# Kernel optimization log

Measured on AMD Instinct MI355X. Metric: run time of the kernel, lower is better.

## Reference

```python
import jax, jax.numpy as jnp
import numpy as np

B, S, D, H = 4, 2048, 1024, 16
HD = D // H
EPS = 1e-5
MASKED_BIAS = -10000.0

def setup_inputs() -> dict:
    key = jax.random.key(0)
    ks = jax.random.split(key, 12)
    sd = 0.02
    return {
        "hidden_states": jax.random.normal(ks[0], (B, S, D), jnp.float32),
        "Wq": jax.random.normal(ks[1], (D, D), jnp.float32) * sd,
        "bq": jnp.zeros((D,), jnp.float32),
        "Wk": jax.random.normal(ks[2], (D, D), jnp.float32) * sd,
        "bk": jnp.zeros((D,), jnp.float32),
        "Wv": jax.random.normal(ks[3], (D, D), jnp.float32) * sd,
        "bv": jnp.zeros((D,), jnp.float32),
        "Wp": jax.random.normal(ks[4], (D, D), jnp.float32) * sd,
        "bp": jnp.zeros((D,), jnp.float32),
        "ln_g": jnp.ones((D,), jnp.float32),
        "ln_b": jnp.zeros((D,), jnp.float32),
    }

def reference(hidden_states, Wq, bq, Wk, bk, Wv, bv, Wp, bp, ln_g, ln_b):
    x = hidden_states  # [B,S,D]
    # QKV projections (nn.Linear: x @ W^T + b; here W stored as [D,D], use x@W)
    q = x @ Wq + bq
    k = x @ Wk + bk
    v = x @ Wv + bv
    # split heads -> [B,H,S,HD]
    def split(t):
        return t.reshape(B, S, H, HD).transpose(0, 2, 1, 3)
    q, k, v = split(q), split(k), split(v)
    # scaled scores [B,H,S,S]
    scores = jnp.einsum("bhqd,bhkd->bhqk", q, k) / jnp.float32(np.sqrt(HD))
    causal = jnp.tril(jnp.ones((S, S), bool))
    scores = jnp.where(causal[None, None], scores, jnp.float32(MASKED_BIAS))
    attn = jax.nn.softmax(scores, axis=-1)
    out = jnp.einsum("bhqk,bhkd->bhqd", attn, v)
    # merge heads -> [B,S,D]
    out = out.transpose(0, 2, 1, 3).reshape(B, S, D)
    out = out @ Wp + bp
    # residual + layernorm
    y = out + x
    mu = jnp.mean(y, axis=-1, keepdims=True)
    var = jnp.var(y, axis=-1, keepdims=True)
    y = (y - mu) * jax.lax.rsqrt(var + EPS) * ln_g + ln_b
    return y
```

## Files before the change

kernel.cpp:

```cpp
#include <hip/hip_runtime.h>
#include <math.h>

#define B_  4
#define S_  2048
#define D_  1024
#define H_  16
#define HD_ 64
#define M_  (B_*S_)

typedef unsigned int  uint;
typedef unsigned short ushort;

typedef __attribute__((ext_vector_type(8))) short bf16x8;
typedef __attribute__((ext_vector_type(4))) float f32x4;

#if __has_builtin(__builtin_amdgcn_exp2f)
#define EXP2(x) __builtin_amdgcn_exp2f(x)
#else
#define EXP2(x) exp2f(x)
#endif

__device__ __forceinline__ ushort f2bf(float x) {
    uint u = __float_as_uint(x);
    u += 0x7FFFu + ((u >> 16) & 1u);
    return (ushort)(u >> 16);
}
__device__ __forceinline__ uint pack2bf(float a, float b) {
    uint ua = __float_as_uint(a); ua += 0x7FFFu + ((ua >> 16) & 1u);
    uint ub = __float_as_uint(b); ub += 0x7FFFu + ((ub >> 16) & 1u);
    return (ua >> 16) | (ub & 0xFFFF0000u);
}

__global__ __launch_bounds__(256) void prep(const float* __restrict__ x,
                                            ushort* __restrict__ xb,
                                            const float* __restrict__ Wq,
                                            const float* __restrict__ Wk,
                                            const float* __restrict__ Wv,
                                            const float* __restrict__ Wp,
                                            ushort* __restrict__ wtq,
                                            ushort* __restrict__ wtk,
                                            ushort* __restrict__ wtv,
                                            ushort* __restrict__ wtp) {
    __shared__ float t[32][33];
    const int tid = threadIdx.x;
    if (blockIdx.z == 0) {
        const int idx = blockIdx.x * 256 + tid;
        const float4* p = (const float4*)(x + (size_t)idx * 8);
        float4 a = p[0], b = p[1];
        uint4 o;
        o.x = pack2bf(a.x, a.y); o.y = pack2bf(a.z, a.w);
        o.z = pack2bf(b.x, b.y); o.w = pack2bf(b.z, b.w);
        ((uint4*)xb)[idx] = o;
    } else {
        const int w = blockIdx.x >> 10;
        const int sub = blockIdx.x & 1023;
        const float* W = (w == 0) ? Wq : (w == 1) ? Wk : (w == 2) ? Wv : Wp;
        ushort* Wt     = (w == 0) ? wtq : (w == 1) ? wtk : (w == 2) ? wtv : wtp;
        const int nb = (sub & 31) * 32, kb = (sub >> 5) * 32;
        #pragma unroll
        for (int l = 0; l < 4; ++l) {
            int idx = tid + l * 256;
            int r = idx >> 5, c = idx & 31;
            t[r][c] = W[(size_t)(kb + r) * D_ + nb + c];
        }
        __syncthreads();
        #pragma unroll
        for (int l = 0; l < 4; ++l) {
            int idx = tid + l * 256;
            int nr = idx >> 5, kc = idx & 31;
            Wt[(size_t)(nb + nr) * D_ + kb + kc] = f2bf(t[kc][nr]);
        }
    }
}

#define GM 128
#define GN 128
#define GK 32

struct GemmLds {
    ushort As[2][GM * GK];
    ushort Bs[2][GN * GK];
};

#define GSTAGE(koff_, buf_) do {                                                \
    _Pragma("unroll")                                                           \
    for (int it_ = 0; it_ < 2; ++it_) {                                         \
        __builtin_amdgcn_global_load_lds(                                       \
            (const __attribute__((address_space(1))) void*)(Ab + (koff_) + sg[it_]), \
            (__attribute__((address_space(3))) void*)(&L.As[buf_][(it_ * 256 + wave * 64) * 8]), 16, 0, 0); \
        __builtin_amdgcn_global_load_lds(                                       \
            (const __attribute__((address_space(1))) void*)(Bb + (koff_) + sg[it_]), \
            (__attribute__((address_space(3))) void*)(&L.Bs[buf_][(it_ * 256 + wave * 64) * 8]), 16, 0, 0); \
    } } while (0)

template <bool SWAP>
__device__ __forceinline__ void gemm_core(GemmLds& L,
                                          const ushort* __restrict__ A,
                                          const ushort* __restrict__ Bt,
                                          f32x4 acc[4][4], int m0, int n0) {
    const int tid  = threadIdx.x;
    const int wave = tid >> 6, lane = tid & 63;
    const int wm = (wave >> 1) * 64, wn = (wave & 1) * 64;
    const int fr = lane & 15, fq = lane >> 4;
    const int xrw = ((fr >> 1) & 3) << 4;

    int sg[2];
    #pragma unroll
    for (int it = 0; it < 2; ++it) {
        const int o = (it * 256 + tid) * 16;
        const int r = o >> 6, c = o & 63;
        sg[it] = r * (D_ * 2) + (c ^ (((r >> 1) & 3) << 4));
    }

    #pragma unroll
    for (int i = 0; i < 4; ++i)
        #pragma unroll
        for (int j = 0; j < 4; ++j) acc[i][j] = (f32x4){0.f, 0.f, 0.f, 0.f};

    const char* Ab = (const char*)A + (size_t)m0 * (D_ * 2);
    const char* Bb = (const char*)Bt + (size_t)n0 * (D_ * 2);

    GSTAGE(0, 0);
    __syncthreads();

    int cur = 0;
    for (int k0 = 0; k0 < D_; k0 += GK) {
        if (k0 + GK < D_) GSTAGE((k0 + GK) * 2, cur ^ 1);

        bf16x8 af[4], bfr[4];
        #pragma unroll
        for (int i = 0; i < 4; ++i)
            af[i] = *(const bf16x8*)((const char*)L.As[cur] + (wm + 16 * i + fr) * 64 + ((fq * 16) ^ xrw));
        #pragma unroll
        for (int j = 0; j < 4; ++j)
            bfr[j] = *(const bf16x8*)((const char*)L.Bs[cur] + (wn + 16 * j + fr) * 64 + ((fq * 16) ^ xrw));
        #pragma unroll
        for (int i = 0; i < 4; ++i)
            #pragma unroll
            for (int j = 0; j < 4; ++j)
                acc[i][j] = SWAP
                    ? __builtin_amdgcn_mfma_f32_16x16x32_bf16(bfr[j], af[i], acc[i][j], 0, 0, 0)
                    : __builtin_amdgcn_mfma_f32_16x16x32_bf16(af[i], bfr[j], acc[i][j], 0, 0, 0);

        __syncthreads();
        cur ^= 1;
    }
}

__global__ __launch_bounds__(256) void gemm_qkvt(const ushort* __restrict__ xb,
                                                 const ushort* __restrict__ wtq,
                                                 const ushort* __restrict__ wtk,
                                                 const ushort* __restrict__ wtv,
                                                 const float* __restrict__ bq,
                                                 const float* __restrict__ bk,
                                                 const float* __restrict__ bv,
                                                 ushort* __restrict__ qb,
                                                 ushort* __restrict__ kb,
                                                 ushort* __restrict__ vtb) {
    __shared__ __align__(16) GemmLds L;
    const int z = blockIdx.z;
    const int lane = threadIdx.x & 63, wave = threadIdx.x >> 6;
    const int wm = (wave >> 1) * 64, wn = (wave & 1) * 64;
    const int cc = lane & 15, fq = lane >> 4;
    const int m0 = blockIdx.x * GM, n0 = blockIdx.y * GN;
    f32x4 acc[4][4];

    if (z < 2) {
        gemm_core<true>(L, xb, z ? wtk : wtq, acc, m0, n0);
        const float* bias = z ? bk : bq;
        ushort* C = z ? kb : qb;
        const float sc = z ? 1.0f : 0.18033688f;
        #pragma unroll
        for (int j = 0; j < 4; ++j) {
            const int f0 = n0 + wn + 16 * j + fq * 4;
            const float4 bs4 = *(const float4*)&bias[f0];
            const int h = f0 >> 6, hd = f0 & 63;
            #pragma unroll
            for (int i = 0; i < 4; ++i) {
                const int token = m0 + wm + 16 * i + cc;
                const int bb = token >> 11, s = token & 2047;
                const float v0 = (acc[i][j][0] + bs4.x) * sc;
                const float v1 = (acc[i][j][1] + bs4.y) * sc;
                const float v2 = (acc[i][j][2] + bs4.z) * sc;
                const float v3 = (acc[i][j][3] + bs4.w) * sc;
                uint2 w; w.x = pack2bf(v0, v1); w.y = pack2bf(v2, v3);
                *(uint2*)&C[(((size_t)bb * H_ + h) * S_ + s) * HD_ + hd] = w;
            }
        }
    } else {
        gemm_core<false>(L, xb, wtv, acc, m0, n0);
        #pragma unroll
        for (int i = 0; i < 4; ++i) {
            const int t0 = m0 + wm + 16 * i + fq * 4;
            const int bb = t0 >> 11, s = t0 & 2047;
            #pragma unroll
            for (int j = 0; j < 4; ++j) {
                const int f = n0 + wn + 16 * j + cc;
                const float bs = bv[f];
                const int h = f >> 6, hd = f & 63;
                uint2 w;
                w.x = pack2bf(acc[i][j][0] + bs, acc[i][j][1] + bs);
                w.y = pack2bf(acc[i][j][2] + bs, acc[i][j][3] + bs);
                *(uint2*)&vtb[(((size_t)bb * H_ + h) * HD_ + hd) * S_ + s] = w;
            }
        }
    }
}

__global__ __launch_bounds__(256) void gemm_p(const ushort* __restrict__ A,
                                              const ushort* __restrict__ Bt,
                                              const float* __restrict__ bias,
                                              float* __restrict__ C) {
    __shared__ __align__(16) GemmLds L;
    const int m0 = blockIdx.y * GM, n0 = blockIdx.x * GN;
    f32x4 acc[4][4];
    gemm_core<false>(L, A, Bt, acc, m0, n0);

    const int lane = threadIdx.x & 63, wave = threadIdx.x >> 6;
    const int wm = (wave >> 1) * 64, wn = (wave & 1) * 64;
    const int cr = (lane >> 4) * 4, cc = lane & 15;
    #pragma unroll
    for (int j = 0; j < 4; ++j) {
        const int col = n0 + wn + 16 * j + cc;
        const float bs = bias[col];
        #pragma unroll
        for (int i = 0; i < 4; ++i)
            #pragma unroll
            for (int r = 0; r < 4; ++r)
                C[(size_t)(m0 + wm + 16 * i + cr + r) * D_ + col] = acc[i][j][r] + bs;
    }
}

#define PST 72

#define STAGE(kt_, buf_) do {                                                   \
    const int kn_ = (kt_) * 64;                                                 \
    __builtin_amdgcn_global_load_lds(                                           \
        (const __attribute__((address_space(1))) void*)((const char*)kbase + (size_t)kn_ * 128 + kg), \
        (__attribute__((address_space(3))) void*)(&Ks[buf_][wave * 512]), 16, 0, 0); \
    __builtin_amdgcn_global_load_lds(                                           \
        (const __attribute__((address_space(1))) void*)((const char*)vbase + (size_t)kn_ * 2 + vg), \
        (__attribute__((address_space(3))) void*)(&Vs[buf_][wave * 512]), 16, 0, 0); \
} while (0)

__global__ __launch_bounds__(512, 4) void attn_mfma(const ushort* __restrict__ qb,
                                                    const ushort* __restrict__ kb,
                                                    const ushort* __restrict__ vtb,
                                                    ushort* __restrict__ ob) {
    __shared__ __align__(16) ushort Ks[2][64 * 64];
    __shared__ __align__(16) ushort Vs[2][64 * 64];
    __shared__ __align__(16) ushort Pp[8][16 * PST];

    const int tid = threadIdx.x, wave = tid >> 6, lane = tid & 63;
    const int fr = lane & 15, fq = lane >> 4;
    const int hb = blockIdx.x;
    const int p  = blockIdx.y;
    const int b = hb >> 4, h = hb & 15;
    const size_t bh = (size_t)b * H_ + h;
    const ushort* qbase = qb + bh * S_ * HD_;
    const ushort* kbase = kb + bh * S_ * HD_;
    const ushort* vbase = vtb + bh * HD_ * S_;
    ushort* PpW = Pp[wave];
    const int xrw = (fr & 7) << 4;

    int kg, vg;
    {
        const int o = tid * 16;
        const int r = o >> 7, cS = o & 127;
        kg = r * 128 + (cS ^ ((r & 7) << 4));
        vg = r * (S_ * 2) + (cS ^ ((r & 7) << 4));
    }

    for (int phase = 0; phase < 2; ++phase) {
        const int chunk = phase ? p : (15 - p);
        const int q0 = chunk * 128;
        const int wq0 = q0 + wave * 16;
        const int qrow = wq0 + fr;
        const int ntile = 2 * (chunk + 1);

        bf16x8 qf[2];
        #pragma unroll
        for (int kk = 0; kk < 2; ++kk)
            qf[kk] = *(const bf16x8*)&qbase[(size_t)qrow * HD_ + kk * 32 + fq * 8];

        f32x4 ot[4];
        #pragma unroll
        for (int mt = 0; mt < 4; ++mt) ot[mt] = (f32x4){0.f, 0.f, 0.f, 0.f};
        float lp = 0.f;

        int cur = 0;
        STAGE(0, 0);
        __syncthreads();

        for (int t = 0; t < ntile; ++t) {
            if (t + 1 < ntile) STAGE(t + 1, cur ^ 1);
            const ushort* Kb = Ks[cur];
            const ushort* Vb = Vs[cur];
            const int k0 = t * 64;

            f32x4 st[4];
            #pragma unroll
            for (int mt = 0; mt < 4; ++mt) st[mt] = (f32x4){0.f, 0.f, 0.f, 0.f};

            if (t < ntile - 2) {
                #pragma unroll
                for (int kk = 0; kk < 2; ++kk) {
                    bf16x8 kf[4];
                    #pragma unroll
                    for (int mt = 0; mt < 4; ++mt)
                        kf[mt] = *(const bf16x8*)((const char*)Kb + (mt * 16 + fr) * 128 + ((kk * 64 + fq * 16) ^ xrw));
                    __builtin_amdgcn_s_setprio(1);
                    #pragma unroll
                    for (int mt = 0; mt < 4; ++mt)
                        st[mt] = __builtin_amdgcn_mfma_f32_16x16x32_bf16(kf[mt], qf[kk], st[mt], 0, 0, 0);
                    __builtin_amdgcn_s_setprio(0);
                }
                #pragma unroll
                for (int mt = 0; mt < 4; ++mt) {
                    float pr[4];
                    #pragma unroll
                    for (int r = 0; r < 4; ++r) pr[r] = EXP2(st[mt][r]);
                    lp += (pr[0] + pr[1]) + (pr[2] + pr[3]);
                    uint2 w;
                    w.x = pack2bf(pr[0], pr[1]);
                    w.y = pack2bf(pr[2], pr[3]);
                    *(uint2*)&PpW[fr * PST + mt * 16 + fq * 4] = w;
                }
                #pragma unroll
                for (int kk = 0; kk < 2; ++kk) {
                    bf16x8 vf[4];
                    #pragma unroll
                    for (int mt = 0; mt < 4; ++mt)
                        vf[mt] = *(const bf16x8*)((const char*)Vb + (mt * 16 + fr) * 128 + ((kk * 64 + fq * 16) ^ xrw));
                    bf16x8 pf = *(const bf16x8*)&PpW[fr * PST + kk * 32 + fq * 8];
                    __builtin_amdgcn_s_setprio(1);
                    #pragma unroll
                    for (int mt = 0; mt < 4; ++mt)
                        ot[mt] = __builtin_amdgcn_mfma_f32_16x16x32_bf16(vf[mt], pf, ot[mt], 0, 0, 0);
                    __builtin_amdgcn_s_setprio(0);
                }
            } else {
                #pragma unroll
                for (int kk = 0; kk < 2; ++kk) {
                    bf16x8 kf[4];
                    #pragma unroll
                    for (int mt = 0; mt < 4; ++mt)
                        kf[mt] = *(const bf16x8*)((const char*)Kb + (mt * 16 + fr) * 128 + ((kk * 64 + fq * 16) ^ xrw));
                    #pragma unroll
                    for (int mt = 0; mt < 4; ++mt)
                        if (k0 + mt * 16 <= wq0 + 15)
                            st[mt] = __builtin_amdgcn_mfma_f32_16x16x32_bf16(kf[mt], qf[kk], st[mt], 0, 0, 0);
                }
                #pragma unroll
                for (int mt = 0; mt < 4; ++mt) {
                    const int kb0 = k0 + mt * 16 + fq * 4;
                    float pr[4];
                    #pragma unroll
                    for (int r = 0; r < 4; ++r) {
                        const float e = EXP2(st[mt][r]);
                        pr[r] = (kb0 + r > qrow) ? 0.f : e;
                    }
                    lp += (pr[0] + pr[1]) + (pr[2] + pr[3]);
                    uint2 w;
                    w.x = pack2bf(pr[0], pr[1]);
                    w.y = pack2bf(pr[2], pr[3]);
                    *(uint2*)&PpW[fr * PST + mt * 16 + fq * 4] = w;
                }
                #pragma unroll
                for (int kk = 0; kk < 2; ++kk) {
                    if (k0 + kk * 32 <= wq0 + 15) {
                        bf16x8 vf[4];
                        #pragma unroll
                        for (int mt = 0; mt < 4; ++mt)
                            vf[mt] = *(const bf16x8*)((const char*)Vb + (mt * 16 + fr) * 128 + ((kk * 64 + fq * 16) ^ xrw));
                        bf16x8 pf = *(const bf16x8*)&PpW[fr * PST + kk * 32 + fq * 8];
                        #pragma unroll
                        for (int mt = 0; mt < 4; ++mt)
                            ot[mt] = __builtin_amdgcn_mfma_f32_16x16x32_bf16(vf[mt], pf, ot[mt], 0, 0, 0);
                    }
                }
            }
            __syncthreads();
            cur ^= 1;
        }

        float l = lp;
        l += __shfl_xor(l, 16);
        l += __shfl_xor(l, 32);
        const float inv = 1.0f / l;
        #pragma unroll
        for (int mt = 0; mt < 4; ++mt) {
            uint2 w;
            w.x = pack2bf(ot[mt][0] * inv, ot[mt][1] * inv);
            w.y = pack2bf(ot[mt][2] * inv, ot[mt][3] * inv);
            *(uint2*)&ob[((size_t)b * S_ + qrow) * D_ + h * HD_ + mt * 16 + fq * 4] = w;
        }
    }
}

__global__ __launch_bounds__(256) void resln(float* __restrict__ out,
                                             const float* __restrict__ x,
                                             const float* __restrict__ g,
                                             const float* __restrict__ bb) {
    __shared__ float red[256];
    const int row = blockIdx.x, tid = threadIdx.x;
    const size_t off = (size_t)row * D_ + tid * 4;

    float4 p  = *(const float4*)&out[off];
    float4 xr = *(const float4*)&x[off];
    float4 y  = make_float4(p.x + xr.x, p.y + xr.y, p.z + xr.z, p.w + xr.w);

    float sum = y.x + y.y + y.z + y.w;
    red[tid] = sum;
    __syncthreads();
    #pragma unroll
    for (int st = 128; st > 0; st >>= 1) {
        if (tid < st) red[tid] += red[tid + st];
        __syncthreads();
    }
    const float mu = red[0] * (1.0f / D_);
    __syncthreads();

    float dx = y.x - mu, dy = y.y - mu, dz = y.z - mu, dw = y.w - mu;
    red[tid] = dx * dx + dy * dy + dz * dz + dw * dw;
    __syncthreads();
    #pragma unroll
    for (int st = 128; st > 0; st >>= 1) {
        if (tid < st) red[tid] += red[tid + st];
        __syncthreads();
    }
    const float var = red[0] * (1.0f / D_);
    const float inv = rsqrtf(var + 1e-5f);

    float4 gg = *(const float4*)&g[tid * 4];
    float4 bv = *(const float4*)&bb[tid * 4];
    float4 r;
    r.x = dx * inv * gg.x + bv.x;
    r.y = dy * inv * gg.y + bv.y;
    r.z = dz * inv * gg.z + bv.z;
    r.w = dw * inv * gg.w + bv.w;
    *(float4*)&out[off] = r;
}

extern "C" void kernel_launch(void* const* d_in, const int* in_sizes, int n_in,
                              void* d_out, int out_size, void* d_ws, size_t ws_size,
                              hipStream_t stream) {
    const float* x    = (const float*)d_in[0];
    const float* Wq   = (const float*)d_in[1];
    const float* bq   = (const float*)d_in[2];
    const float* Wk   = (const float*)d_in[3];
    const float* bk   = (const float*)d_in[4];
    const float* Wv   = (const float*)d_in[5];
    const float* bv   = (const float*)d_in[6];
    const float* Wp   = (const float*)d_in[7];
    const float* bp   = (const float*)d_in[8];
    const float* ln_g = (const float*)d_in[9];
    const float* ln_b = (const float*)d_in[10];

    float* out = (float*)d_out;

    char* ws = (char*)d_ws;
    ushort* qb  = (ushort*)ws;
    ushort* kb  = (ushort*)(ws + (size_t)16 * (1 << 20));
    ushort* vtb = (ushort*)(ws + (size_t)32 * (1 << 20));
    ushort* xb  = (ushort*)(ws + (size_t)48 * (1 << 20));
    ushort* ob  = (ushort*)(ws + (size_t)64 * (1 << 20));
    ushort* wtq = (ushort*)(ws + (size_t)80 * (1 << 20));
    ushort* wtk = (ushort*)(ws + (size_t)82 * (1 << 20));
    ushort* wtv = (ushort*)(ws + (size_t)84 * (1 << 20));
    ushort* wtp = (ushort*)(ws + (size_t)86 * (1 << 20));

    prep<<<dim3(4096, 1, 2), 256, 0, stream>>>(x, xb, Wq, Wk, Wv, Wp, wtq, wtk, wtv, wtp);

    gemm_qkvt<<<dim3(M_ / GM, D_ / GN, 3), 256, 0, stream>>>(
        xb, wtq, wtk, wtv, bq, bk, bv, qb, kb, vtb);

    attn_mfma<<<dim3(64, 8), 512, 0, stream>>>(qb, kb, vtb, ob);

    gemm_p<<<dim3(D_ / GN, M_ / GM), 256, 0, stream>>>(ob, wtp, bp, out);
    resln<<<M_, 256, 0, stream>>>(out, x, ln_g, ln_b);
}
```

Measured before the change: 280.6 us.

## Triple-buffer LDS staging with one barrier per tile in GEMM and attention

```diff
diff --git a/kernel.cpp b/kernel.cpp
--- a/kernel.cpp
+++ b/kernel.cpp
@@ -78,8 +78,8 @@
 #define GK 32
 
 struct GemmLds {
-    ushort As[2][GM * GK];
-    ushort Bs[2][GN * GK];
+    ushort As[3][GM * GK];
+    ushort Bs[3][GN * GK];
 };
 
 #define GSTAGE(koff_, buf_) do {                                                \
@@ -120,20 +120,25 @@
     const char* Ab = (const char*)A + (size_t)m0 * (D_ * 2);
     const char* Bb = (const char*)Bt + (size_t)n0 * (D_ * 2);
 
+    const int NT = D_ / GK;
     GSTAGE(0, 0);
-    __syncthreads();
-
-    int cur = 0;
-    for (int k0 = 0; k0 < D_; k0 += GK) {
-        if (k0 + GK < D_) GSTAGE((k0 + GK) * 2, cur ^ 1);
-
+    GSTAGE(GK * 2, 1);
+
+    for (int t = 0; t < NT; ++t) {
+        if (t + 1 < NT) { asm volatile("s_waitcnt vmcnt(4)" ::: "memory"); }
+        else            { asm volatile("s_waitcnt vmcnt(0)" ::: "memory"); }
+        __builtin_amdgcn_s_barrier();
+        if (t + 2 < NT) GSTAGE((t + 2) * (GK * 2), (t + 2) % 3);
+
+        const char* As_ = (const char*)L.As[t % 3];
+        const char* Bs_ = (const char*)L.Bs[t % 3];
         bf16x8 af[4], bfr[4];
         #pragma unroll
         for (int i = 0; i < 4; ++i)
-            af[i] = *(const bf16x8*)((const char*)L.As[cur] + (wm + 16 * i + fr) * 64 + ((fq * 16) ^ xrw));
+            af[i] = *(const bf16x8*)(As_ + (wm + 16 * i + fr) * 64 + ((fq * 16) ^ xrw));
         #pragma unroll
         for (int j = 0; j < 4; ++j)
-            bfr[j] = *(const bf16x8*)((const char*)L.Bs[cur] + (wn + 16 * j + fr) * 64 + ((fq * 16) ^ xrw));
+            bfr[j] = *(const bf16x8*)(Bs_ + (wn + 16 * j + fr) * 64 + ((fq * 16) ^ xrw));
         #pragma unroll
         for (int i = 0; i < 4; ++i)
             #pragma unroll
@@ -141,9 +146,6 @@
                 acc[i][j] = SWAP
                     ? __builtin_amdgcn_mfma_f32_16x16x32_bf16(bfr[j], af[i], acc[i][j], 0, 0, 0)
                     : __builtin_amdgcn_mfma_f32_16x16x32_bf16(af[i], bfr[j], acc[i][j], 0, 0, 0);
-
-        __syncthreads();
-        cur ^= 1;
     }
 }
 
@@ -247,8 +249,8 @@
                                                     const ushort* __restrict__ kb,
                                                     const ushort* __restrict__ vtb,
                                                     ushort* __restrict__ ob) {
-    __shared__ __align__(16) ushort Ks[2][64 * 64];
-    __shared__ __align__(16) ushort Vs[2][64 * 64];
+    __shared__ __align__(16) ushort Ks[3][64 * 64];
+    __shared__ __align__(16) ushort Vs[3][64 * 64];
     __shared__ __align__(16) ushort Pp[8][16 * PST];
 
     const int tid = threadIdx.x, wave = tid >> 6, lane = tid & 63;
@@ -288,14 +290,17 @@
         for (int mt = 0; mt < 4; ++mt) ot[mt] = (f32x4){0.f, 0.f, 0.f, 0.f};
         float lp = 0.f;
 
-        int cur = 0;
         STAGE(0, 0);
-        __syncthreads();
+        if (ntile > 1) STAGE(1, 1);
 
         for (int t = 0; t < ntile; ++t) {
-            if (t + 1 < ntile) STAGE(t + 1, cur ^ 1);
-            const ushort* Kb = Ks[cur];
-            const ushort* Vb = Vs[cur];
+            if (t + 1 < ntile) { asm volatile("s_waitcnt vmcnt(2)" ::: "memory"); }
+            else               { asm volatile("s_waitcnt vmcnt(0)" ::: "memory"); }
+            __builtin_amdgcn_s_barrier();
+            if (t + 2 < ntile) STAGE(t + 2, (t + 2) % 3);
+
+            const ushort* Kb = Ks[t % 3];
+            const ushort* Vb = Vs[t % 3];
             const int k0 = t * 64;
 
             f32x4 st[4];
@@ -380,9 +385,8 @@
                     }
                 }
             }
-            __syncthreads();
-            cur ^= 1;
-        }
+        }
+        __syncthreads();
 
         float l = lp;
         l += __shfl_xor(l, 16);
```

Result: no change. 282.1 us (+0.5%).

## Triple-buffer GEMM LDS staging with vmcnt-based waits and one barrier per step

Applied to the files above, without the earlier changes.

```diff
diff --git a/kernel.cpp b/kernel.cpp
--- a/kernel.cpp
+++ b/kernel.cpp
@@ -78,8 +78,8 @@
 #define GK 32
 
 struct GemmLds {
-    ushort As[2][GM * GK];
-    ushort Bs[2][GN * GK];
+    ushort As[3][GM * GK];
+    ushort Bs[3][GN * GK];
 };
 
 #define GSTAGE(koff_, buf_) do {                                                \
@@ -93,6 +93,32 @@
             (__attribute__((address_space(3))) void*)(&L.Bs[buf_][(it_ * 256 + wave * 64) * 8]), 16, 0, 0); \
     } } while (0)
 
+#define GCOMP(BUF_) do {                                                        \
+    const char* As_ = (const char*)L.As[BUF_];                                  \
+    const char* Bs_ = (const char*)L.Bs[BUF_];                                  \
+    bf16x8 af[4], bfr[4];                                                       \
+    _Pragma("unroll")                                                           \
+    for (int i_ = 0; i_ < 4; ++i_)                                              \
+        af[i_] = *(const bf16x8*)(As_ + (wm + 16 * i_ + fr) * 64 + ((fq * 16) ^ xrw)); \
+    _Pragma("unroll")                                                           \
+    for (int j_ = 0; j_ < 4; ++j_)                                              \
+        bfr[j_] = *(const bf16x8*)(Bs_ + (wn + 16 * j_ + fr) * 64 + ((fq * 16) ^ xrw)); \
+    _Pragma("unroll")                                                           \
+    for (int i_ = 0; i_ < 4; ++i_)                                              \
+        _Pragma("unroll")                                                       \
+        for (int j_ = 0; j_ < 4; ++j_)                                          \
+            acc[i_][j_] = SWAP                                                  \
+                ? __builtin_amdgcn_mfma_f32_16x16x32_bf16(bfr[j_], af[i_], acc[i_][j_], 0, 0, 0) \
+                : __builtin_amdgcn_mfma_f32_16x16x32_bf16(af[i_], bfr[j_], acc[i_][j_], 0, 0, 0); \
+    } while (0)
+
+#define GSTEP(BUF_, SBUF_, SOFF_) do {                                          \
+    asm volatile("s_waitcnt vmcnt(4)" ::: "memory");                            \
+    __builtin_amdgcn_s_barrier();                                               \
+    GSTAGE(SOFF_, SBUF_);                                                       \
+    GCOMP(BUF_);                                                                \
+    } while (0)
+
 template <bool SWAP>
 __device__ __forceinline__ void gemm_core(GemmLds& L,
                                           const ushort* __restrict__ A,
@@ -121,30 +147,19 @@
     const char* Bb = (const char*)Bt + (size_t)n0 * (D_ * 2);
 
     GSTAGE(0, 0);
-    __syncthreads();
-
-    int cur = 0;
-    for (int k0 = 0; k0 < D_; k0 += GK) {
-        if (k0 + GK < D_) GSTAGE((k0 + GK) * 2, cur ^ 1);
-
-        bf16x8 af[4], bfr[4];
-        #pragma unroll
-        for (int i = 0; i < 4; ++i)
-            af[i] = *(const bf16x8*)((const char*)L.As[cur] + (wm + 16 * i + fr) * 64 + ((fq * 16) ^ xrw));
-        #pragma unroll
-        for (int j = 0; j < 4; ++j)
-            bfr[j] = *(const bf16x8*)((const char*)L.Bs[cur] + (wn + 16 * j + fr) * 64 + ((fq * 16) ^ xrw));
-        #pragma unroll
-        for (int i = 0; i < 4; ++i)
-            #pragma unroll
-            for (int j = 0; j < 4; ++j)
-                acc[i][j] = SWAP
-                    ? __builtin_amdgcn_mfma_f32_16x16x32_bf16(bfr[j], af[i], acc[i][j], 0, 0, 0)
-                    : __builtin_amdgcn_mfma_f32_16x16x32_bf16(af[i], bfr[j], acc[i][j], 0, 0, 0);
-
-        __syncthreads();
-        cur ^= 1;
-    }
+    GSTAGE(64, 1);
+
+    for (int t = 0; t < 30; t += 3) {
+        GSTEP(0, 2, (t + 2) * 64);
+        GSTEP(1, 0, (t + 3) * 64);
+        GSTEP(2, 1, (t + 4) * 64);
+    }
+    asm volatile("s_waitcnt vmcnt(4)" ::: "memory");
+    __builtin_amdgcn_s_barrier();
+    GCOMP(0);
+    asm volatile("s_waitcnt vmcnt(0)" ::: "memory");
+    __builtin_amdgcn_s_barrier();
+    GCOMP(1);
 }
 
 __global__ __launch_bounds__(256) void gemm_qkvt(const ushort* __restrict__ xb,
```

Result: no change. 277.1 us (-1.3%).

## Restructure QKV GEMM with 128x256 tiles, 8 waves and triple-buffered pipeline

Applied to the files above, without the earlier changes.

```diff
diff --git a/kernel.cpp b/kernel.cpp
--- a/kernel.cpp
+++ b/kernel.cpp
@@ -19,6 +19,9 @@
 #else
 #define EXP2(x) exp2f(x)
 #endif
+
+#define GPTR(p) (const __attribute__((address_space(1))) void*)(p)
+#define LPTR(p) (__attribute__((address_space(3))) void*)(p)
 
 __device__ __forceinline__ ushort f2bf(float x) {
     uint u = __float_as_uint(x);
@@ -73,43 +76,70 @@
     }
 }
 
-#define GM 128
-#define GN 128
-#define GK 32
-
-struct GemmLds {
-    ushort As[2][GM * GK];
-    ushort Bs[2][GN * GK];
+struct QLds {
+    ushort As[3][128 * 32];
+    ushort Bs[3][256 * 32];
 };
 
-#define GSTAGE(koff_, buf_) do {                                                \
+#define QSTAGE(tile_, buf_) do {                                                \
+    const int ko_ = (tile_) * 64;                                               \
+    __builtin_amdgcn_global_load_lds(GPTR(Ab + ko_ + sgA),                      \
+        LPTR(&L.As[buf_][wave * 512]), 16, 0, 0);                               \
+    __builtin_amdgcn_global_load_lds(GPTR(Bb + ko_ + sgB0),                     \
+        LPTR(&L.Bs[buf_][wave * 512]), 16, 0, 0);                               \
+    __builtin_amdgcn_global_load_lds(GPTR(Bb + ko_ + sgB1),                     \
+        LPTR(&L.Bs[buf_][4096 + wave * 512]), 16, 0, 0);                        \
+} while (0)
+
+#define QCOMPUTE(buf_) do {                                                     \
+    const char* As_ = (const char*)L.As[buf_];                                  \
+    const char* Bs_ = (const char*)L.Bs[buf_];                                  \
+    bf16x8 af[4], bf[4];                                                        \
     _Pragma("unroll")                                                           \
-    for (int it_ = 0; it_ < 2; ++it_) {                                         \
-        __builtin_amdgcn_global_load_lds(                                       \
-            (const __attribute__((address_space(1))) void*)(Ab + (koff_) + sg[it_]), \
-            (__attribute__((address_space(3))) void*)(&L.As[buf_][(it_ * 256 + wave * 64) * 8]), 16, 0, 0); \
-        __builtin_amdgcn_global_load_lds(                                       \
-            (const __attribute__((address_space(1))) void*)(Bb + (koff_) + sg[it_]), \
-            (__attribute__((address_space(3))) void*)(&L.Bs[buf_][(it_ * 256 + wave * 64) * 8]), 16, 0, 0); \
-    } } while (0)
+    for (int i_ = 0; i_ < 4; ++i_)                                              \
+        af[i_] = *(const bf16x8*)(As_ + (wm + 16 * i_ + fr) * 64 + ((fq * 16) ^ xrw)); \
+    _Pragma("unroll")                                                           \
+    for (int j_ = 0; j_ < 4; ++j_)                                              \
+        bf[j_] = *(const bf16x8*)(Bs_ + (wn + 16 * j_ + fr) * 64 + ((fq * 16) ^ xrw)); \
+    __builtin_amdgcn_s_setprio(1);                                              \
+    _Pragma("unroll")                                                           \
+    for (int i_ = 0; i_ < 4; ++i_)                                              \
+        _Pragma("unroll")                                                       \
+        for (int j_ = 0; j_ < 4; ++j_)                                          \
+            acc[i_][j_] = SWAP                                                  \
+                ? __builtin_amdgcn_mfma_f32_16x16x32_bf16(bf[j_], af[i_], acc[i_][j_], 0, 0, 0) \
+                : __builtin_amdgcn_mfma_f32_16x16x32_bf16(af[i_], bf[j_], acc[i_][j_], 0, 0, 0); \
+    __builtin_amdgcn_s_setprio(0);                                              \
+} while (0)
+
+#define QSTEP(buf_, sbuf_, stile_) do {                                         \
+    asm volatile("s_waitcnt vmcnt(3)" ::: "memory");                            \
+    __builtin_amdgcn_s_barrier();                                               \
+    QSTAGE(stile_, sbuf_);                                                      \
+    QCOMPUTE(buf_);                                                             \
+} while (0)
 
 template <bool SWAP>
-__device__ __forceinline__ void gemm_core(GemmLds& L,
-                                          const ushort* __restrict__ A,
-                                          const ushort* __restrict__ Bt,
-                                          f32x4 acc[4][4], int m0, int n0) {
+__device__ __forceinline__ void qcore(QLds& L,
+                                      const ushort* __restrict__ A,
+                                      const ushort* __restrict__ Bt,
+                                      f32x4 acc[4][4], int m0, int n0) {
     const int tid  = threadIdx.x;
     const int wave = tid >> 6, lane = tid & 63;
-    const int wm = (wave >> 1) * 64, wn = (wave & 1) * 64;
+    const int wm = (wave >> 2) * 64;
+    const int wn = (wave & 3) * 64;
     const int fr = lane & 15, fq = lane >> 4;
     const int xrw = ((fr >> 1) & 3) << 4;
 
-    int sg[2];
-    #pragma unroll
-    for (int it = 0; it < 2; ++it) {
-        const int o = (it * 256 + tid) * 16;
-        const int r = o >> 6, c = o & 63;
-        sg[it] = r * (D_ * 2) + (c ^ (((r >> 1) & 3) << 4));
+    int sgA, sgB0, sgB1;
+    {
+        int o = tid * 16;
+        int r = o >> 6, c = o & 63;
+        sgA = r * (D_ * 2) + (c ^ (((r >> 1) & 3) << 4));
+        sgB0 = sgA;
+        o = 8192 + tid * 16;
+        r = o >> 6; c = o & 63;
+        sgB1 = r * (D_ * 2) + (c ^ (((r >> 1) & 3) << 4));
     }
 
     #pragma unroll
@@ -120,53 +150,44 @@
     const char* Ab = (const char*)A + (size_t)m0 * (D_ * 2);
     const char* Bb = (const char*)Bt + (size_t)n0 * (D_ * 2);
 
-    GSTAGE(0, 0);
-    __syncthreads();
-
-    int cur = 0;
-    for (int k0 = 0; k0 < D_; k0 += GK) {
-        if (k0 + GK < D_) GSTAGE((k0 + GK) * 2, cur ^ 1);
-
-        bf16x8 af[4], bfr[4];
-        #pragma unroll
-        for (int i = 0; i < 4; ++i)
-            af[i] = *(const bf16x8*)((const char*)L.As[cur] + (wm + 16 * i + fr) * 64 + ((fq * 16) ^ xrw));
-        #pragma unroll
-        for (int j = 0; j < 4; ++j)
-            bfr[j] = *(const bf16x8*)((const char*)L.Bs[cur] + (wn + 16 * j + fr) * 64 + ((fq * 16) ^ xrw));
-        #pragma unroll
-        for (int i = 0; i < 4; ++i)
-            #pragma unroll
-            for (int j = 0; j < 4; ++j)
-                acc[i][j] = SWAP
-                    ? __builtin_amdgcn_mfma_f32_16x16x32_bf16(bfr[j], af[i], acc[i][j], 0, 0, 0)
-                    : __builtin_amdgcn_mfma_f32_16x16x32_bf16(af[i], bfr[j], acc[i][j], 0, 0, 0);
-
-        __syncthreads();
-        cur ^= 1;
-    }
-}
-
-__global__ __launch_bounds__(256) void gemm_qkvt(const ushort* __restrict__ xb,
-                                                 const ushort* __restrict__ wtq,
-                                                 const ushort* __restrict__ wtk,
-                                                 const ushort* __restrict__ wtv,
-                                                 const float* __restrict__ bq,
-                                                 const float* __restrict__ bk,
-                                                 const float* __restrict__ bv,
-                                                 ushort* __restrict__ qb,
-                                                 ushort* __restrict__ kb,
-                                                 ushort* __restrict__ vtb) {
-    __shared__ __align__(16) GemmLds L;
+    QSTAGE(0, 0);
+    QSTAGE(1, 1);
+
+    #pragma unroll 1
+    for (int it = 0; it < 10; ++it) {
+        const int t0 = it * 3;
+        QSTEP(0, 2, t0 + 2);
+        QSTEP(1, 0, t0 + 3);
+        QSTEP(2, 1, t0 + 4);
+    }
+    asm volatile("s_waitcnt vmcnt(3)" ::: "memory");
+    __builtin_amdgcn_s_barrier();
+    QCOMPUTE(0);
+    asm volatile("s_waitcnt vmcnt(0)" ::: "memory");
+    __builtin_amdgcn_s_barrier();
+    QCOMPUTE(1);
+}
+
+__global__ __launch_bounds__(512, 4) void gemm_qkvt(const ushort* __restrict__ xb,
+                                                    const ushort* __restrict__ wtq,
+                                                    const ushort* __restrict__ wtk,
+                                                    const ushort* __restrict__ wtv,
+                                                    const float* __restrict__ bq,
+                                                    const float* __restrict__ bk,
+                                                    const float* __restrict__ bv,
+                                                    ushort* __restrict__ qb,
+                                                    ushort* __restrict__ kb,
+                                                    ushort* __restrict__ vtb) {
+    __shared__ __align__(16) QLds L;
     const int z = blockIdx.z;
     const int lane = threadIdx.x & 63, wave = threadIdx.x >> 6;
-    const int wm = (wave >> 1) * 64, wn = (wave & 1) * 64;
+    const int wm = (wave >> 2) * 64, wn = (wave & 3) * 64;
     const int cc = lane & 15, fq = lane >> 4;
-    const int m0 = blockIdx.x * GM, n0 = blockIdx.y * GN;
+    const int m0 = blockIdx.x * 128, n0 = blockIdx.y * 256;
     f32x4 acc[4][4];
 
     if (z < 2) {
-        gemm_core<true>(L, xb, z ? wtk : wtq, acc, m0, n0);
+        qcore<true>(L, xb, z ? wtk : wtq, acc, m0, n0);
         const float* bias = z ? bk : bq;
         ushort* C = z ? kb : qb;
         const float sc = z ? 1.0f : 0.18033688f;
@@ -188,7 +209,7 @@
             }
         }
     } else {
-        gemm_core<false>(L, xb, wtv, acc, m0, n0);
+        qcore<false>(L, xb, wtv, acc, m0, n0);
         #pragma unroll
         for (int i = 0; i < 4; ++i) {
             const int t0 = m0 + wm + 16 * i + fq * 4;
@@ -207,14 +228,83 @@
     }
 }
 
+#define GM 128
+#define GN 128
+#define GK 32
+
+struct PLds {
+    ushort As[2][GM * GK];
+    ushort Bs[2][GN * GK];
+};
+
+#define PSTAGE(koff_, buf_) do {                                                \
+    _Pragma("unroll")                                                           \
+    for (int it_ = 0; it_ < 2; ++it_) {                                         \
+        __builtin_amdgcn_global_load_lds(GPTR(Ab + (koff_) + sg[it_]),          \
+            LPTR(&L.As[buf_][(it_ * 256 + wave * 64) * 8]), 16, 0, 0);          \
+        __builtin_amdgcn_global_load_lds(GPTR(Bb + (koff_) + sg[it_]),          \
+            LPTR(&L.Bs[buf_][(it_ * 256 + wave * 64) * 8]), 16, 0, 0);          \
+    } } while (0)
+
+__device__ __forceinline__ void pgemm_core(PLds& L,
+                                           const ushort* __restrict__ A,
+                                           const ushort* __restrict__ Bt,
+                                           f32x4 acc[4][4], int m0, int n0) {
+    const int tid  = threadIdx.x;
+    const int wave = tid >> 6, lane = tid & 63;
+    const int wm = (wave >> 1) * 64, wn = (wave & 1) * 64;
+    const int fr = lane & 15, fq = lane >> 4;
+    const int xrw = ((fr >> 1) & 3) << 4;
+
+    int sg[2];
+    #pragma unroll
+    for (int it = 0; it < 2; ++it) {
+        const int o = (it * 256 + tid) * 16;
+        const int r = o >> 6, c = o & 63;
+        sg[it] = r * (D_ * 2) + (c ^ (((r >> 1) & 3) << 4));
+    }
+
+    #pragma unroll
+    for (int i = 0; i < 4; ++i)
+        #pragma unroll
+        for (int j = 0; j < 4; ++j) acc[i][j] = (f32x4){0.f, 0.f, 0.f, 0.f};
+
+    const char* Ab = (const char*)A + (size_t)m0 * (D_ * 2);
+    const char* Bb = (const char*)Bt + (size_t)n0 * (D_ * 2);
+
+    PSTAGE(0, 0);
+    __syncthreads();
+
+    int cur = 0;
+    for (int k0 = 0; k0 < D_; k0 += GK) {
+        if (k0 + GK < D_) PSTAGE((k0 + GK) * 2, cur ^ 1);
+
+        bf16x8 af[4], bfr[4];
+        #pragma unroll
+        for (int i = 0; i < 4; ++i)
+            af[i] = *(const bf16x8*)((const char*)L.As[cur] + (wm + 16 * i + fr) * 64 + ((fq * 16) ^ xrw));
+        #pragma unroll
+        for (int j = 0; j < 4; ++j)
+            bfr[j] = *(const bf16x8*)((const char*)L.Bs[cur] + (wn + 16 * j + fr) * 64 + ((fq * 16) ^ xrw));
+        #pragma unroll
+        for (int i = 0; i < 4; ++i)
+            #pragma unroll
+            for (int j = 0; j < 4; ++j)
+                acc[i][j] = __builtin_amdgcn_mfma_f32_16x16x32_bf16(af[i], bfr[j], acc[i][j], 0, 0, 0);
+
+        __syncthreads();
+        cur ^= 1;
+    }
+}
+
 __global__ __launch_bounds__(256) void gemm_p(const ushort* __restrict__ A,
                                               const ushort* __restrict__ Bt,
                                               const float* __restrict__ bias,
                                               float* __restrict__ C) {
-    __shared__ __align__(16) GemmLds L;
+    __shared__ __align__(16) PLds L;
     const int m0 = blockIdx.y * GM, n0 = blockIdx.x * GN;
     f32x4 acc[4][4];
-    gemm_core<false>(L, A, Bt, acc, m0, n0);
+    pgemm_core(L, A, Bt, acc, m0, n0);
 
     const int lane = threadIdx.x & 63, wave = threadIdx.x >> 6;
     const int wm = (wave >> 1) * 64, wn = (wave & 1) * 64;
@@ -236,11 +326,11 @@
 #define STAGE(kt_, buf_) do {                                                   \
     const int kn_ = (kt_) * 64;                                                 \
     __builtin_amdgcn_global_load_lds(                                           \
-        (const __attribute__((address_space(1))) void*)((const char*)kbase + (size_t)kn_ * 128 + kg), \
-        (__attribute__((address_space(3))) void*)(&Ks[buf_][wave * 512]), 16, 0, 0); \
+        GPTR((const char*)kbase + (size_t)kn_ * 128 + kg),                      \
+        LPTR(&Ks[buf_][wave * 512]), 16, 0, 0);                                 \
     __builtin_amdgcn_global_load_lds(                                           \
-        (const __attribute__((address_space(1))) void*)((const char*)vbase + (size_t)kn_ * 2 + vg), \
-        (__attribute__((address_space(3))) void*)(&Vs[buf_][wave * 512]), 16, 0, 0); \
+        GPTR((const char*)vbase + (size_t)kn_ * 2 + vg),                        \
+        LPTR(&Vs[buf_][wave * 512]), 16, 0, 0);                                 \
 } while (0)
 
 __global__ __launch_bounds__(512, 4) void attn_mfma(const ushort* __restrict__ qb,
@@ -472,7 +562,7 @@
 
     prep<<<dim3(4096, 1, 2), 256, 0, stream>>>(x, xb, Wq, Wk, Wv, Wp, wtq, wtk, wtv, wtp);
 
-    gemm_qkvt<<<dim3(M_ / GM, D_ / GN, 3), 256, 0, stream>>>(
+    gemm_qkvt<<<dim3(M_ / 128, D_ / 256, 3), 512, 0, stream>>>(
         xb, wtq, wtk, wtv, bq, bk, bv, qb, kb, vtb);
 
     attn_mfma<<<dim3(64, 8), 512, 0, stream>>>(qb, kb, vtb, ob);
```

New measurement: 286.4 us. 1.02x slower.
